# Optimization experiments

Hardware: AMD Instinct MI355X
Metric: run time of the kernel (lower is better)

The kernel has to match this reference:

```python
import jax, jax.numpy as jnp
import numpy as np

D_MODEL = 1024
NUM_HEADS = 16
D_K = D_MODEL // NUM_HEADS
D_FF = 4096
B, S = 4, 2048
EPS = 1e-5


def _linear_params(key, d_in, d_out):
    # torch nn.Linear default init: U(-1/sqrt(d_in), 1/sqrt(d_in))
    k1, k2 = jax.random.split(key)
    bound = 1.0 / np.sqrt(d_in)
    W = jax.random.uniform(k1, (d_in, d_out), jnp.float32, -bound, bound)
    b = jax.random.uniform(k2, (d_out,), jnp.float32, -bound, bound)
    return W, b


def setup_inputs() -> dict:
    key = jax.random.key(0)
    ks = jax.random.split(key, 8)
    x = jax.random.normal(ks[0], (B, S, D_MODEL), jnp.float32)
    Wq, bq = _linear_params(ks[1], D_MODEL, D_MODEL)
    Wk, bk = _linear_params(ks[2], D_MODEL, D_MODEL)
    Wv, bv = _linear_params(ks[3], D_MODEL, D_MODEL)
    Wo, bo = _linear_params(ks[4], D_MODEL, D_MODEL)
    W1, b1 = _linear_params(ks[5], D_MODEL, D_FF)
    W2, b2 = _linear_params(ks[6], D_FF, D_MODEL)
    ln1_g = jnp.ones((D_MODEL,), jnp.float32)
    ln1_b = jnp.zeros((D_MODEL,), jnp.float32)
    ln2_g = jnp.ones((D_MODEL,), jnp.float32)
    ln2_b = jnp.zeros((D_MODEL,), jnp.float32)
    return dict(x=x, Wq=Wq, bq=bq, Wk=Wk, bk=bk, Wv=Wv, bv=bv, Wo=Wo, bo=bo,
                W1=W1, b1=b1, W2=W2, b2=b2,
                ln1_g=ln1_g, ln1_b=ln1_b, ln2_g=ln2_g, ln2_b=ln2_b)


def _layernorm(x, g, b):
    mu = jnp.mean(x, axis=-1, keepdims=True)
    var = jnp.mean(jnp.square(x - mu), axis=-1, keepdims=True)
    return (x - mu) * jax.lax.rsqrt(var + EPS) * g + b


def _attention(h, Wq, bq, Wk, bk, Wv, bv, Wo, bo):
    b, s, _ = h.shape
    def split_heads(t):  # (b,s,d) -> (b,H,s,dk)
        return t.reshape(b, s, NUM_HEADS, D_K).transpose(0, 2, 1, 3)
    Q = split_heads(h @ Wq + bq)
    K = split_heads(h @ Wk + bk)
    V = split_heads(h @ Wv + bv)
    scores = jnp.einsum('bhqd,bhkd->bhqk', Q, K) / np.sqrt(D_K)
    causal = jnp.tril(jnp.ones((s, s), dtype=bool))  # True = keep
    scores = jnp.where(causal, scores, -jnp.inf)
    attn = jax.nn.softmax(scores, axis=-1)
    out = jnp.einsum('bhqk,bhkd->bhqd', attn, V)
    out = out.transpose(0, 2, 1, 3).reshape(b, s, D_MODEL)
    return out @ Wo + bo


def reference(x, Wq, bq, Wk, bk, Wv, bv, Wo, bo, W1, b1, W2, b2,
              ln1_g, ln1_b, ln2_g, ln2_b):
    # pre-norm residual block
    x = x + _attention(_layernorm(x, ln1_g, ln1_b), Wq, bq, Wk, bk, Wv, bv, Wo, bo)
    h = _layernorm(x, ln2_g, ln2_b)
    x = x + (jax.nn.relu(h @ W1 + b1) @ W2 + b2)
    return x
```

## Files before the change

### kernel.cpp

```cpp
#include <hip/hip_runtime.h>
#include <hip/hip_bf16.h>

typedef __bf16 bf16;
typedef __attribute__((ext_vector_type(8))) __bf16 bf16x8;
typedef __attribute__((ext_vector_type(4))) float f32x4;

#define D_MODEL 1024
#define NHEADS  16
#define DK      64
#define DFF     4096
#define BATCH   4
#define SEQ     2048
#define NTOK    (BATCH*SEQ)
#define QSCALE  0.18033688011112042f

__device__ __forceinline__ void gload16(const bf16* g, bf16* l) {
    __builtin_amdgcn_global_load_lds((const __attribute__((address_space(1))) void*)g,
                                     (__attribute__((address_space(3))) void*)l, 16, 0, 0);
}

__global__ __launch_bounds__(256) void transpose_cast4(
    const float* __restrict__ W0, const float* __restrict__ W1,
    const float* __restrict__ W2, const float* __restrict__ W3,
    bf16* __restrict__ T0, bf16* __restrict__ T1,
    bf16* __restrict__ T2, bf16* __restrict__ T3)
{
    const int z = blockIdx.z;
    const float* W = (z == 0) ? W0 : (z == 1) ? W1 : (z == 2) ? W2 : W3;
    bf16*       Wt = (z == 0) ? T0 : (z == 1) ? T1 : (z == 2) ? T2 : T3;
    const int K = 1024, N = 1024;
    __shared__ float tile[32][33];
    const int tx = threadIdx.x, ty = threadIdx.y;
    const int n0 = blockIdx.x * 32, k0 = blockIdx.y * 32;
#pragma unroll
    for (int i = 0; i < 4; ++i)
        tile[ty + i*8][tx] = W[(size_t)(k0 + ty + i*8) * N + n0 + tx];
    __syncthreads();
#pragma unroll
    for (int i = 0; i < 4; ++i)
        Wt[(size_t)(n0 + ty + i*8) * K + k0 + tx] = (bf16)tile[tx][ty + i*8];
}

__global__ __launch_bounds__(256) void transpose_cast(
    const float* __restrict__ W, bf16* __restrict__ Wt, int K, int N)
{
    __shared__ float tile[32][33];
    const int tx = threadIdx.x, ty = threadIdx.y;
    const int n0 = blockIdx.x * 32, k0 = blockIdx.y * 32;
#pragma unroll
    for (int i = 0; i < 4; ++i)
        tile[ty + i*8][tx] = W[(size_t)(k0 + ty + i*8) * N + n0 + tx];
    __syncthreads();
#pragma unroll
    for (int i = 0; i < 4; ++i)
        Wt[(size_t)(n0 + ty + i*8) * K + k0 + tx] = (bf16)tile[tx][ty + i*8];
}

__global__ __launch_bounds__(256) void transpose_v(
    const bf16* __restrict__ V, bf16* __restrict__ VT)
{
    __shared__ bf16 t[64][72];
    const int bh = blockIdx.y;
    const int s0 = blockIdx.x * 64;
    const int r  = threadIdx.x >> 2;
    const int c0 = (threadIdx.x & 3) * 16;
    const bf16* Vb = V  + (size_t)bh * SEQ * DK;
    bf16*       Tb = VT + (size_t)bh * DK * SEQ;
#pragma unroll
    for (int i = 0; i < 2; ++i) {
        bf16x8 v = *(const bf16x8*)&Vb[(size_t)(s0 + r) * DK + c0 + i*8];
#pragma unroll
        for (int j = 0; j < 8; ++j) t[c0 + i*8 + j][r] = v[j];
    }
    __syncthreads();
#pragma unroll
    for (int i = 0; i < 2; ++i) {
        bf16x8 o;
#pragma unroll
        for (int j = 0; j < 8; ++j) o[j] = t[r][c0 + i*8 + j];
        *(bf16x8*)&Tb[(size_t)r * SEQ + s0 + c0 + i*8] = o;
    }
}

__global__ __launch_bounds__(256) void ln_kernel(
    const float* __restrict__ x, const float* __restrict__ g,
    const float* __restrict__ beta, bf16* __restrict__ out)
{
    const int row = blockIdx.x, tid = threadIdx.x;
    const f32x4* xr = (const f32x4*)(x + (size_t)row * D_MODEL);
    f32x4 v = xr[tid];
    float s  = v[0] + v[1] + v[2] + v[3];
    float s2 = v[0]*v[0] + v[1]*v[1] + v[2]*v[2] + v[3]*v[3];
#pragma unroll
    for (int off = 32; off > 0; off >>= 1) {
        s  += __shfl_down(s,  off, 64);
        s2 += __shfl_down(s2, off, 64);
    }
    __shared__ float red[8];
    const int wave = tid >> 6, lane = tid & 63;
    if (lane == 0) { red[wave] = s; red[wave + 4] = s2; }
    __syncthreads();
    if (tid == 0) {
        float a = red[0] + red[1] + red[2] + red[3];
        float c = red[4] + red[5] + red[6] + red[7];
        float mu  = a * (1.0f / D_MODEL);
        float var = c * (1.0f / D_MODEL) - mu * mu;
        red[0] = mu;
        red[1] = rsqrtf(var + 1e-5f);
    }
    __syncthreads();
    const float mu = red[0], rs = red[1];
    f32x4 gv = ((const f32x4*)g)[tid];
    f32x4 bv = ((const f32x4*)beta)[tid];
    union { bf16 h[4]; uint2 u; } o;
#pragma unroll
    for (int i = 0; i < 4; ++i) o.h[i] = (bf16)((v[i] - mu) * rs * gv[i] + bv[i]);
    *(uint2*)(out + (size_t)row * D_MODEL + tid * 4) = o.u;
}

template<int EPI>
__global__ __launch_bounds__(256, 2) void gemm_bf16(
    const bf16* __restrict__ A, const bf16* __restrict__ Bt,
    const float* __restrict__ bias, const float* __restrict__ bias2,
    const float* __restrict__ bias3, const float* __restrict__ resid,
    void* __restrict__ outp, int M, int N, int K)
{
    __shared__ __align__(16) bf16 As[128 * 32];
    __shared__ __align__(16) bf16 Bs[128 * 32];
    const int tid  = threadIdx.x;
    const int wave = tid >> 6, lane = tid & 63;
    const int quad = lane >> 4, l16 = lane & 15;
    const int wr = wave >> 1, wc = wave & 1;
    const int m0 = blockIdx.x * 128, n0 = blockIdx.y * 128;

    const int r0 = wave * 32 + (lane >> 2);
    const int r1 = r0 + 16;
    const int u0 = ((lane & 3) - ((r0 >> 1) & 3)) & 3;
    const int u1 = ((lane & 3) - ((r1 >> 1) & 3)) & 3;
    const bf16* gA0 = A  + (size_t)(m0 + r0) * K + u0 * 8;
    const bf16* gA1 = A  + (size_t)(m0 + r1) * K + u1 * 8;
    const bf16* gB0 = Bt + (size_t)(n0 + r0) * K + u0 * 8;
    const bf16* gB1 = Bt + (size_t)(n0 + r1) * K + u1 * 8;
    bf16* lA0 = As + wave * 1024;
    bf16* lA1 = As + wave * 1024 + 512;
    bf16* lB0 = Bs + wave * 1024;
    bf16* lB1 = Bs + wave * 1024 + 512;

    int aoff[4], boff[4];
#pragma unroll
    for (int i = 0; i < 4; ++i) {
        const int ra = wr * 64 + i * 16 + l16;
        aoff[i] = ra * 32 + ((quad + ((ra >> 1) & 3)) & 3) * 8;
        const int rb = wc * 64 + i * 16 + l16;
        boff[i] = rb * 32 + ((quad + ((rb >> 1) & 3)) & 3) * 8;
    }

    const f32x4 vzero = {0.f, 0.f, 0.f, 0.f};
    f32x4 acc[4][4];
#pragma unroll
    for (int i = 0; i < 4; ++i)
#pragma unroll
        for (int j = 0; j < 4; ++j) acc[i][j] = vzero;

    for (int k0 = 0; k0 < K; k0 += 32) {
        __syncthreads();
        gload16(gA0 + k0, lA0);
        gload16(gA1 + k0, lA1);
        gload16(gB0 + k0, lB0);
        gload16(gB1 + k0, lB1);
        __syncthreads();
        bf16x8 af[4], bfr[4];
#pragma unroll
        for (int i = 0; i < 4; ++i) af[i]  = *(const bf16x8*)&As[aoff[i]];
#pragma unroll
        for (int j = 0; j < 4; ++j) bfr[j] = *(const bf16x8*)&Bs[boff[j]];
#pragma unroll
        for (int i = 0; i < 4; ++i)
#pragma unroll
            for (int j = 0; j < 4; ++j)
                acc[i][j] = __builtin_amdgcn_mfma_f32_16x16x32_bf16(af[i], bfr[j], acc[i][j], 0, 0, 0);
    }

#pragma unroll
    for (int i = 0; i < 4; ++i) {
#pragma unroll
        for (int j = 0; j < 4; ++j) {
            const int col = n0 + wc * 64 + j * 16 + l16;
            float bcol, sc = 1.0f;
            if (EPI == 0) {
                const int seg = col >> 10;
                const float* bp = (seg == 0) ? bias : ((seg == 1) ? bias2 : bias3);
                bcol = bp[col & 1023];
                if (seg == 0) sc = QSCALE;
            } else {
                bcol = bias[col];
            }
#pragma unroll
            for (int r = 0; r < 4; ++r) {
                const int row = m0 + wr * 64 + i * 16 + quad * 4 + r;
                const float v = acc[i][j][r] + bcol;
                if (EPI == 0) {
                    const int bb = row >> 11, ss = row & (SEQ - 1);
                    const int hh = (col & 1023) >> 6, dd = col & (DK - 1);
                    const size_t seg = (size_t)(col >> 10);
                    ((bf16*)outp)[seg * 8388608 + (((size_t)(bb * NHEADS + hh)) * SEQ + ss) * DK + dd] = (bf16)(v * sc);
                } else if (EPI == 1) {
                    const size_t idx = (size_t)row * N + col;
                    ((float*)outp)[idx] = v + resid[idx];
                } else {
                    ((bf16*)outp)[(size_t)row * N + col] = (bf16)fmaxf(v, 0.f);
                }
            }
        }
    }
}

__global__ __launch_bounds__(256, 2) void attn_kernel(
    const bf16* __restrict__ Q, const bf16* __restrict__ K,
    const bf16* __restrict__ VT, bf16* __restrict__ out)
{
    const int bh = blockIdx.x;
    const int b = bh >> 4, h = bh & 15;
    const int tid  = threadIdx.x;
    const int wave = tid >> 6, lane = tid & 63;
    const int quad = lane >> 4, l16 = lane & 15;

    __shared__ __align__(16) bf16 smem[32768 + 4 * 1152];
    bf16* Pw = smem + 32768 + wave * 1152;

    const bf16* Qb = Q  + (size_t)bh * SEQ * DK;
    const bf16* Kb = K  + (size_t)bh * SEQ * DK;
    const bf16* Vb = VT + (size_t)bh * DK * SEQ;

    int goK[4], goV[4], lo[4];
#pragma unroll
    for (int i = 0; i < 4; ++i) {
        const int U = (wave * 4 + i) * 64 + lane;
        const int rK = U >> 3, uK = (U & 7) ^ (rK & 7);
        goK[i] = rK * DK + uK * 8;
        const int rV = U >> 4, usw = U & 15;
        const int uV = (usw & 8) | ((usw & 7) ^ (rV & 7));
        goV[i] = rV * SEQ + uV * 8;
        lo[i]  = (wave * 4 + i) * 512;
    }

    auto stage = [&](int buf, int t) {
        const bf16* kp = Kb + (size_t)(t * 128) * DK;
        const bf16* vp = Vb + t * 128;
        bf16* kb = smem + buf * 8192;
        bf16* vb = smem + 16384 + buf * 8192;
#pragma unroll
        for (int i = 0; i < 4; ++i) gload16(kp + goK[i], kb + lo[i]);
#pragma unroll
        for (int i = 0; i < 4; ++i) gload16(vp + goV[i], vb + lo[i]);
    };

    const f32x4 vzero = {0.f, 0.f, 0.f, 0.f};
    int g = 0;
    stage(0, 0);

    for (int phase = 0; phase < 2; ++phase) {
        const int qt = phase ? (int)blockIdx.y : 15 - (int)blockIdx.y;
        const int qw = qt * 128 + wave * 32;

        bf16x8 qf[2][2];
#pragma unroll
        for (int qi = 0; qi < 2; ++qi)
#pragma unroll
            for (int kk = 0; kk < 2; ++kk)
                qf[qi][kk] = *(const bf16x8*)&Qb[(size_t)(qw + qi*16 + l16) * DK + kk*32 + quad*8];

        f32x4 Oacc[2][4];
        float m_[2], l_[2];
#pragma unroll
        for (int qi = 0; qi < 2; ++qi) {
            m_[qi] = -1.0e30f; l_[qi] = 0.f;
#pragma unroll
            for (int dj = 0; dj < 4; ++dj) Oacc[qi][dj] = vzero;
        }

        for (int t = 0; t <= qt; ++t, ++g) {
            const int cur = g & 1;
            __syncthreads();
            if (t < qt)            stage(cur ^ 1, t + 1);
            else if (phase == 0)   stage(cur ^ 1, 0);
            const bf16* kb = smem + cur * 8192;
            const bf16* vb = smem + 16384 + cur * 8192;
            const int kv0 = t * 128;

            f32x4 sv[8][2];
#pragma unroll
            for (int kvt = 0; kvt < 8; ++kvt) {
                const int R = kvt*16 + l16, rx = R & 7;
                bf16x8 kf0 = *(const bf16x8*)&kb[R*64 + (quad ^ rx)*8];
                bf16x8 kf1 = *(const bf16x8*)&kb[R*64 + (((quad + 4) & 7) ^ rx)*8];
#pragma unroll
                for (int qi = 0; qi < 2; ++qi) {
                    f32x4 tacc = vzero;
                    tacc = __builtin_amdgcn_mfma_f32_16x16x32_bf16(kf0, qf[qi][0], tacc, 0, 0, 0);
                    tacc = __builtin_amdgcn_mfma_f32_16x16x32_bf16(kf1, qf[qi][1], tacc, 0, 0, 0);
                    sv[kvt][qi] = tacc;
                }
            }

            if (t == qt) {
#pragma unroll
                for (int kvt = 0; kvt < 8; ++kvt)
#pragma unroll
                    for (int qi = 0; qi < 2; ++qi)
#pragma unroll
                        for (int r = 0; r < 4; ++r) {
                            const int kv = kv0 + kvt*16 + quad*4 + r;
                            const int q  = qw + qi*16 + l16;
                            if (kv > q) sv[kvt][qi][r] = -1.0e30f;
                        }
            }

#pragma unroll
            for (int qi = 0; qi < 2; ++qi) {
                float mx = sv[0][qi][0];
#pragma unroll
                for (int kvt = 0; kvt < 8; ++kvt)
#pragma unroll
                    for (int r = 0; r < 4; ++r) mx = fmaxf(mx, sv[kvt][qi][r]);
                mx = fmaxf(mx, __shfl_xor(mx, 16, 64));
                mx = fmaxf(mx, __shfl_xor(mx, 32, 64));
                const float newm  = fmaxf(m_[qi], mx);
                const float alpha = exp2f(m_[qi] - newm);
                m_[qi] = newm;
                float rs = 0.f;
#pragma unroll
                for (int kvt = 0; kvt < 8; ++kvt)
#pragma unroll
                    for (int r = 0; r < 4; ++r) {
                        const float p = exp2f(sv[kvt][qi][r] - newm);
                        sv[kvt][qi][r] = p;
                        rs += p;
                    }
                rs += __shfl_xor(rs, 16, 64);
                rs += __shfl_xor(rs, 32, 64);
                l_[qi] = l_[qi] * alpha + rs;
#pragma unroll
                for (int dj = 0; dj < 4; ++dj) Oacc[qi][dj] *= alpha;
            }

#pragma unroll
            for (int c2 = 0; c2 < 4; ++c2) {
#pragma unroll
                for (int qi = 0; qi < 2; ++qi)
#pragma unroll
                    for (int kl = 0; kl < 2; ++kl) {
                        union { bf16 h[4]; unsigned long long u; } pk;
                        const f32x4 s = sv[c2*2 + kl][qi];
#pragma unroll
                        for (int r = 0; r < 4; ++r) pk.h[r] = (bf16)s[r];
                        *(unsigned long long*)&Pw[(qi*16 + l16)*36 + kl*16 + quad*4] = pk.u;
                    }
                bf16x8 vf[4];
#pragma unroll
                for (int dj = 0; dj < 4; ++dj) {
                    const int R = dj*16 + l16;
                    const int u = c2*4 + quad;
                    const int usw = (u & 8) | ((u & 7) ^ (R & 7));
                    vf[dj] = *(const bf16x8*)&vb[R*128 + usw*8];
                }
#pragma unroll
                for (int qi = 0; qi < 2; ++qi) {
                    bf16x8 pf = *(const bf16x8*)&Pw[(qi*16 + l16)*36 + quad*8];
#pragma unroll
                    for (int dj = 0; dj < 4; ++dj)
                        Oacc[qi][dj] = __builtin_amdgcn_mfma_f32_16x16x32_bf16(vf[dj], pf, Oacc[qi][dj], 0, 0, 0);
                }
            }
        }

        const float inv0 = 1.0f / l_[0], inv1 = 1.0f / l_[1];
#pragma unroll
        for (int dh = 0; dh < 2; ++dh) {
#pragma unroll
            for (int qi = 0; qi < 2; ++qi) {
                const float inv = qi ? inv1 : inv0;
#pragma unroll
                for (int djl = 0; djl < 2; ++djl) {
                    const int dj = dh*2 + djl;
                    union { bf16 h[4]; unsigned long long u; } ok;
#pragma unroll
                    for (int r = 0; r < 4; ++r) ok.h[r] = (bf16)(Oacc[qi][dj][r] * inv);
                    *(unsigned long long*)&Pw[(qi*16 + l16)*36 + djl*16 + quad*4] = ok.u;
                }
            }
            const int row = lane >> 1;
#pragma unroll
            for (int it = 0; it < 2; ++it) {
                const int grp = (lane & 1) + 2*it;
                bf16x8 o = *(const bf16x8*)&Pw[row*36 + grp*8];
                *(bf16x8*)&out[((size_t)(b*SEQ + qw - wave*32 + wave*32 + row))*D_MODEL + h*DK + dh*32 + grp*8] = o;
            }
        }
    }
}

extern "C" void kernel_launch(void* const* d_in, const int* in_sizes, int n_in,
                              void* d_out, int out_size, void* d_ws, size_t ws_size,
                              hipStream_t stream)
{
    const float* x    = (const float*)d_in[0];
    const float* Wq   = (const float*)d_in[1];
    const float* bq   = (const float*)d_in[2];
    const float* Wk   = (const float*)d_in[3];
    const float* bk   = (const float*)d_in[4];
    const float* Wv   = (const float*)d_in[5];
    const float* bv   = (const float*)d_in[6];
    const float* Wo   = (const float*)d_in[7];
    const float* bo   = (const float*)d_in[8];
    const float* W1   = (const float*)d_in[9];
    const float* b1   = (const float*)d_in[10];
    const float* W2   = (const float*)d_in[11];
    const float* b2   = (const float*)d_in[12];
    const float* ln1g = (const float*)d_in[13];
    const float* ln1b = (const float*)d_in[14];
    const float* ln2g = (const float*)d_in[15];
    const float* ln2b = (const float*)d_in[16];

    char* ws = (char*)d_ws;
    const size_t MB = 1024 * 1024;
    bf16* WTq  = (bf16*)(ws + 0 * MB);
    bf16* WTk  = (bf16*)(ws + 2 * MB);
    bf16* WTv  = (bf16*)(ws + 4 * MB);
    bf16* WTo  = (bf16*)(ws + 6 * MB);
    bf16* WT1  = (bf16*)(ws + 8 * MB);
    bf16* WT2  = (bf16*)(ws + 16 * MB);
    bf16* hbuf = (bf16*)(ws + 24 * MB);
    bf16* VhT  = (bf16*)(ws + 24 * MB);
    bf16* Qh   = (bf16*)(ws + 40 * MB);
    bf16* Kh   = (bf16*)(ws + 56 * MB);
    bf16* Vh   = (bf16*)(ws + 72 * MB);
    bf16* attn = (bf16*)(ws + 88 * MB);
    bf16* ff1  = (bf16*)(ws + 40 * MB);
    float* x2  = (float*)d_out;

    dim3 tb(32, 8);
    transpose_cast4<<<dim3(32, 32, 4), tb, 0, stream>>>(Wq, Wk, Wv, Wo, WTq, WTk, WTv, WTo);
    transpose_cast<<<dim3(128, 32), tb, 0, stream>>>(W1, WT1, 1024, 4096);
    transpose_cast<<<dim3(32, 128), tb, 0, stream>>>(W2, WT2, 4096, 1024);

    ln_kernel<<<NTOK, 256, 0, stream>>>(x, ln1g, ln1b, hbuf);

    gemm_bf16<0><<<dim3(64, 24), 256, 0, stream>>>(hbuf, WTq, bq, bk, bv, nullptr, Qh, NTOK, 3072, 1024);

    transpose_v<<<dim3(32, 64), 256, 0, stream>>>(Vh, VhT);

    attn_kernel<<<dim3(64, 8), 256, 0, stream>>>(Qh, Kh, VhT, attn);

    gemm_bf16<1><<<dim3(64, 8), 256, 0, stream>>>(attn, WTo, bo, nullptr, nullptr, x, x2, NTOK, 1024, 1024);

    ln_kernel<<<NTOK, 256, 0, stream>>>(x2, ln2g, ln2b, hbuf);

    gemm_bf16<2><<<dim3(64, 32), 256, 0, stream>>>(hbuf, WT1, b1, nullptr, nullptr, nullptr, ff1, NTOK, 4096, 1024);
    gemm_bf16<1><<<dim3(64, 8),  256, 0, stream>>>(ff1, WT2, b2, nullptr, nullptr, x2, x2, NTOK, 1024, 4096);
}
```

Measured before the change: 518.8 us.

## Add 256x256-tile 512-thread GEMM with phased LDS pipeline for QKV and FFN

Introduces a new gemm256 kernel that computes 256x256 output tiles with 8 waves and 4x4 MFMA fragments per wave. It double-buffers K-tiles split into two halves, issuing async global-to-LDS loads interleaved with four MFMA phases, with setprio and barriers to overlap memory and compute. The QKV, FFN1 and FFN2 GEMMs switch to it, which raises operand reuse per block and cuts global traffic. The trade-off is fewer blocks: FFN2 launches only 128 blocks on a device with many more CUs, plus heavier register use and 128KB of shared memory per block.

```diff
diff --git a/kernel.cpp b/kernel.cpp
--- a/kernel.cpp
+++ b/kernel.cpp
@@ -199,6 +199,160 @@
             for (int r = 0; r < 4; ++r) {
                 const int row = m0 + wr * 64 + i * 16 + quad * 4 + r;
                 const float v = acc[i][j][r] + bcol;
+                if (EPI == 0) {
+                    const int bb = row >> 11, ss = row & (SEQ - 1);
+                    const int hh = (col & 1023) >> 6, dd = col & (DK - 1);
+                    const size_t seg = (size_t)(col >> 10);
+                    ((bf16*)outp)[seg * 8388608 + (((size_t)(bb * NHEADS + hh)) * SEQ + ss) * DK + dd] = (bf16)(v * sc);
+                } else if (EPI == 1) {
+                    const size_t idx = (size_t)row * N + col;
+                    ((float*)outp)[idx] = v + resid[idx];
+                } else {
+                    ((bf16*)outp)[(size_t)row * N + col] = (bf16)fmaxf(v, 0.f);
+                }
+            }
+        }
+    }
+}
+
+#define PH_WAIT() do { \
+    __builtin_amdgcn_s_barrier(); \
+    asm volatile("s_waitcnt lgkmcnt(0)" ::: "memory"); \
+    __builtin_amdgcn_sched_barrier(0); \
+} while (0)
+
+template<int EPI>
+__global__ __launch_bounds__(512, 2) void gemm256(
+    const bf16* __restrict__ A, const bf16* __restrict__ Bt,
+    const float* __restrict__ bias, const float* __restrict__ bias2,
+    const float* __restrict__ bias3, const float* __restrict__ resid,
+    void* __restrict__ outp, int M, int N, int K)
+{
+    __shared__ __align__(16) bf16 smem[65536];
+    const int tid  = threadIdx.x;
+    const int wave = tid >> 6, lane = tid & 63;
+    const int quad = lane >> 4, l16 = lane & 15;
+    const int wr = wave >> 2, wcn = wave & 3;
+    const int m0 = blockIdx.x * 256, n0 = blockIdx.y * 256;
+    const int NT = K >> 6;
+
+    const bf16* gA[2]; const bf16* gB[2]; int ldsOff[2];
+#pragma unroll
+    for (int l = 0; l < 2; ++l) {
+        const int slot = tid + l * 512;
+        const int r = slot >> 2;
+        const int clog = (slot & 3) ^ ((r >> 1) & 3);
+        gA[l] = A  + (size_t)(m0 + r) * K + clog * 8;
+        gB[l] = Bt + (size_t)(n0 + r) * K + clog * 8;
+        ldsOff[l] = (wave * 64 + l * 512) * 8;
+    }
+
+    auto stageA = [&](int buf, int t, int kk) {
+        bf16* dst = smem + (buf * 2 + kk) * 8192;
+#pragma unroll
+        for (int l = 0; l < 2; ++l) gload16(gA[l] + t * 64 + kk * 32, dst + ldsOff[l]);
+    };
+    auto stageB = [&](int buf, int t, int kk) {
+        bf16* dst = smem + 32768 + (buf * 2 + kk) * 8192;
+#pragma unroll
+        for (int l = 0; l < 2; ++l) gload16(gB[l] + t * 64 + kk * 32, dst + ldsOff[l]);
+    };
+
+    const int cswz  = (quad ^ ((l16 >> 1) & 3)) * 8;
+    const int aBase = (wr * 128 + l16) * 32 + cswz;
+    const int bBase = (wcn * 64 + l16) * 32 + cswz;
+
+    f32x4 acc[8][4];
+    const f32x4 vzero = {0.f, 0.f, 0.f, 0.f};
+#pragma unroll
+    for (int i = 0; i < 8; ++i)
+#pragma unroll
+        for (int j = 0; j < 4; ++j) acc[i][j] = vzero;
+
+    stageA(0, 0, 0); stageB(0, 0, 0);
+    stageA(0, 0, 1); stageB(0, 0, 1);
+    if (NT > 1) {
+        stageA(1, 1, 0); stageB(1, 1, 0);
+        asm volatile("s_waitcnt vmcnt(4)" ::: "memory");
+    } else {
+        asm volatile("s_waitcnt vmcnt(0)" ::: "memory");
+    }
+    __builtin_amdgcn_s_barrier();
+
+    bf16x8 af[4], bfr[4];
+#define GMM_MFMA(mh) do { \
+    __builtin_amdgcn_s_setprio(1); \
+    _Pragma("unroll") \
+    for (int i_ = 0; i_ < 4; ++i_) { \
+        _Pragma("unroll") \
+        for (int j_ = 0; j_ < 4; ++j_) \
+            acc[(mh)*4 + i_][j_] = __builtin_amdgcn_mfma_f32_16x16x32_bf16(af[i_], bfr[j_], acc[(mh)*4 + i_][j_], 0, 0, 0); \
+    } \
+    __builtin_amdgcn_s_setprio(0); \
+    __builtin_amdgcn_s_barrier(); \
+} while (0)
+
+#pragma unroll 1
+    for (int t = 0; t < NT; ++t) {
+        const int buf = t & 1;
+        const bf16* As0 = smem + buf * 16384;
+        const bf16* As1 = As0 + 8192;
+        const bf16* Bs0 = smem + 32768 + buf * 16384;
+        const bf16* Bs1 = Bs0 + 8192;
+
+#pragma unroll
+        for (int i = 0; i < 4; ++i) af[i]  = *(const bf16x8*)&As0[aBase + i * 512];
+#pragma unroll
+        for (int j = 0; j < 4; ++j) bfr[j] = *(const bf16x8*)&Bs0[bBase + j * 512];
+        if (t + 1 < NT) stageA(buf ^ 1, t + 1, 1);
+        PH_WAIT();
+        GMM_MFMA(0);
+
+#pragma unroll
+        for (int i = 0; i < 4; ++i) af[i] = *(const bf16x8*)&As0[aBase + 2048 + i * 512];
+        if (t + 1 < NT) stageB(buf ^ 1, t + 1, 1);
+        PH_WAIT();
+        GMM_MFMA(1);
+
+#pragma unroll
+        for (int i = 0; i < 4; ++i) af[i]  = *(const bf16x8*)&As1[aBase + 2048 + i * 512];
+#pragma unroll
+        for (int j = 0; j < 4; ++j) bfr[j] = *(const bf16x8*)&Bs1[bBase + j * 512];
+        if (t + 2 < NT) stageA(buf, t + 2, 0);
+        PH_WAIT();
+        GMM_MFMA(1);
+
+#pragma unroll
+        for (int i = 0; i < 4; ++i) af[i] = *(const bf16x8*)&As1[aBase + i * 512];
+        if (t + 2 < NT) {
+            stageB(buf, t + 2, 0);
+            asm volatile("s_waitcnt vmcnt(4)" ::: "memory");
+        } else {
+            asm volatile("s_waitcnt vmcnt(0)" ::: "memory");
+        }
+        PH_WAIT();
+        GMM_MFMA(0);
+    }
+#undef GMM_MFMA
+
+#pragma unroll
+    for (int mf = 0; mf < 8; ++mf) {
+#pragma unroll
+        for (int nf = 0; nf < 4; ++nf) {
+            const int col = n0 + wcn * 64 + nf * 16 + l16;
+            float bcol, sc = 1.0f;
+            if (EPI == 0) {
+                const int seg = col >> 10;
+                const float* bp = (seg == 0) ? bias : ((seg == 1) ? bias2 : bias3);
+                bcol = bp[col & 1023];
+                if (seg == 0) sc = QSCALE;
+            } else {
+                bcol = bias[col];
+            }
+#pragma unroll
+            for (int r = 0; r < 4; ++r) {
+                const int row = m0 + wr * 128 + mf * 16 + quad * 4 + r;
+                const float v = acc[mf][nf][r] + bcol;
                 if (EPI == 0) {
                     const int bb = row >> 11, ss = row & (SEQ - 1);
                     const int hh = (col & 1023) >> 6, dd = col & (DK - 1);
@@ -446,7 +600,7 @@
 
     ln_kernel<<<NTOK, 256, 0, stream>>>(x, ln1g, ln1b, hbuf);
 
-    gemm_bf16<0><<<dim3(64, 24), 256, 0, stream>>>(hbuf, WTq, bq, bk, bv, nullptr, Qh, NTOK, 3072, 1024);
+    gemm256<0><<<dim3(32, 12), 512, 0, stream>>>(hbuf, WTq, bq, bk, bv, nullptr, Qh, NTOK, 3072, 1024);
 
     transpose_v<<<dim3(32, 64), 256, 0, stream>>>(Vh, VhT);
 
@@ -456,6 +610,6 @@
 
     ln_kernel<<<NTOK, 256, 0, stream>>>(x2, ln2g, ln2b, hbuf);
 
-    gemm_bf16<2><<<dim3(64, 32), 256, 0, stream>>>(hbuf, WT1, b1, nullptr, nullptr, nullptr, ff1, NTOK, 4096, 1024);
-    gemm_bf16<1><<<dim3(64, 8),  256, 0, stream>>>(ff1, WT2, b2, nullptr, nullptr, x2, x2, NTOK, 1024, 4096);
-}
+    gemm256<2><<<dim3(32, 16), 512, 0, stream>>>(hbuf, WT1, b1, nullptr, nullptr, nullptr, ff1, NTOK, 4096, 1024);
+    gemm256<1><<<dim3(32, 4), 512, 0, stream>>>(ff1, WT2, b2, nullptr, nullptr, x2, x2, NTOK, 1024, 4096);
+}
```

New measurement: 526.6 us. About the same (+1.5%).
